# Kernel optimization log

Measured on AMD Instinct MI355X. Metric: run time of the kernel, lower is better.

## Reference

```python
import jax, jax.numpy as jnp
import numpy as np

B, T, C = 4, 2048, 1024
H, DH = 16, 64  # head_count, per-head dim = head_size // head_count


def setup_inputs() -> dict:
    key = jax.random.key(0)
    ks = jax.random.split(key, 5)
    s = 1.0 / np.sqrt(C)
    return {
        "x": jax.random.normal(ks[0], (B, T, C), dtype=jnp.float32),
        "Wq": jax.random.normal(ks[1], (H, C, DH), dtype=jnp.float32) * s,
        "Wk": jax.random.normal(ks[2], (H, C, DH), dtype=jnp.float32) * s,
        "Wv": jax.random.normal(ks[3], (H, C, DH), dtype=jnp.float32) * s,
        "Wproj": jax.random.normal(ks[4], (C, C), dtype=jnp.float32) * s,
    }


def reference(x, Wq, Wk, Wv, Wproj):
    b, t, c = x.shape
    q = jnp.einsum("btc,hcd->bhtd", x, Wq)
    k = jnp.einsum("btc,hcd->bhtd", x, Wk)
    v = jnp.einsum("btc,hcd->bhtd", x, Wv)
    # NOTE: source scales by embed_size**-0.5, not head_dim**-0.5
    wei = jnp.einsum("bhtd,bhsd->bhts", q, k) * (c ** -0.5)
    causal = jnp.tril(jnp.ones((t, t), dtype=bool))
    wei = jnp.where(causal, wei, jnp.finfo(wei.dtype).min)
    wei = jax.nn.softmax(wei, axis=-1)
    out = jnp.einsum("bhts,bhsd->bhtd", wei, v)
    out = out.transpose(0, 2, 1, 3).reshape(b, t, -1)  # concat heads -> [B,T,H*DH]
    return out @ Wproj
```

## Files before the change

kernel.cpp:

```cpp
#include <hip/hip_runtime.h>
#include <math.h>
#include <stdint.h>

#define BB 4
#define TT 2048
#define CC 1024
#define HH 16
#define DH 64
#define BT (BB*TT)
#define NQKV (3*HH*DH)

typedef __attribute__((ext_vector_type(8))) __bf16 bf16x8;
typedef __attribute__((ext_vector_type(4))) float f32x4;
typedef __attribute__((ext_vector_type(16))) float f32x16;
typedef __attribute__((ext_vector_type(8))) unsigned short u16x8;
typedef __attribute__((ext_vector_type(4))) unsigned int u32x4;

__device__ __forceinline__ unsigned short f2b(float f) {
  union { float f; unsigned u; } v; v.f = f;
  unsigned r = v.u + 0x7fffu + ((v.u >> 16) & 1u);
  return (unsigned short)(r >> 16);
}

__device__ __forceinline__ void gload_lds16(const void* g, void* lds) {
  __builtin_amdgcn_global_load_lds(
      (const __attribute__((address_space(1))) void*)(uintptr_t)g,
      (__attribute__((address_space(3))) void*)(uintptr_t)lds, 16, 0, 0);
}

__device__ __forceinline__ unsigned cvtpk_bf16(float lo, float hi) {
  unsigned r;
  asm("v_cvt_pk_bf16_f32 %0, %1, %2" : "=v"(r) : "v"(lo), "v"(hi));
  return r;
}

__device__ __forceinline__ float fexp2(float x) {
#if __has_builtin(__builtin_amdgcn_exp2f)
  return __builtin_amdgcn_exp2f(x);
#else
  float r; asm("v_exp_f32 %0, %1" : "=v"(r) : "v"(x)); return r;
#endif
}

__global__ __launch_bounds__(256) void cvt_bf16(const float* __restrict__ in,
                                                unsigned short* __restrict__ out, int n) {
  int i = (blockIdx.x * 256 + threadIdx.x) * 8;
  if (i + 8 > n) return;
  float4 a = *(const float4*)(in + i);
  float4 b = *(const float4*)(in + i + 4);
  u16x8 pk;
  pk[0] = f2b(a.x); pk[1] = f2b(a.y); pk[2] = f2b(a.z); pk[3] = f2b(a.w);
  pk[4] = f2b(b.x); pk[5] = f2b(b.y); pk[6] = f2b(b.z); pk[7] = f2b(b.w);
  *(u16x8*)(out + i) = pk;
}

__global__ __launch_bounds__(256) void transpose_cvt(const float* __restrict__ in,
                                                     unsigned short* __restrict__ out,
                                                     int R, int Cc) {
  __shared__ float tile[32][33];
  const int z = blockIdx.z;
  in  += (size_t)z * R * Cc;
  out += (size_t)z * R * Cc;
  const int r0 = blockIdx.y * 32, c0 = blockIdx.x * 32;
  const int tx = threadIdx.x, ty = threadIdx.y;
  #pragma unroll
  for (int i = 0; i < 32; i += 8)
    tile[ty + i][tx] = in[(size_t)(r0 + ty + i) * Cc + c0 + tx];
  __syncthreads();
  #pragma unroll
  for (int i = 0; i < 32; i += 8)
    out[(size_t)(c0 + ty + i) * R + r0 + tx] = f2b(tile[tx][ty + i]);
}

template<int MODE>
__global__ __launch_bounds__(256) void mfma_gemm(
    const unsigned short* __restrict__ A,
    const unsigned short* __restrict__ Bt,
    void* __restrict__ Cout, int M, int N, int K)
{
  __shared__ unsigned short As[128 * 32];
  __shared__ unsigned short Bs[128 * 32];
  const int tid = threadIdx.x;
  const int l = tid & 63, w = tid >> 6;
  const int wr = w >> 1, wc = w & 1;
  const long row0 = (long)blockIdx.x * 128, col0 = (long)blockIdx.y * 128;

  const int srow = tid >> 2;
  const int skoff = (tid & 3) * 8;
  const unsigned short* Ap = A + (row0 + srow) * (long)K + skoff;
  const unsigned short* Bp = Bt + (col0 + srow) * (long)K + skoff;
  char* AsB = (char*)As + (size_t)w * 1024;
  char* BsB = (char*)Bs + (size_t)w * 1024;

  f32x4 acc[4][4];
  #pragma unroll
  for (int i = 0; i < 4; ++i)
    #pragma unroll
    for (int j = 0; j < 4; ++j) acc[i][j] = (f32x4){0.f, 0.f, 0.f, 0.f};

  const int fr = l & 15, fg = l >> 4;
  const unsigned short* aBase = As + (wr * 64 + fr) * 32 + fg * 8;
  const unsigned short* bBase = Bs + (wc * 64 + fr) * 32 + fg * 8;

  for (int k0 = 0; k0 < K; k0 += 32) {
    gload_lds16(Ap + k0, AsB);
    gload_lds16(Ap + 64 * (long)K + k0, AsB + 4096);
    gload_lds16(Bp + k0, BsB);
    gload_lds16(Bp + 64 * (long)K + k0, BsB + 4096);
    __syncthreads();
    bf16x8 af[4], bfr[4];
    #pragma unroll
    for (int m = 0; m < 4; ++m) af[m] = *(const bf16x8*)(aBase + m * 16 * 32);
    #pragma unroll
    for (int n = 0; n < 4; ++n) bfr[n] = *(const bf16x8*)(bBase + n * 16 * 32);
    #pragma unroll
    for (int m = 0; m < 4; ++m)
      #pragma unroll
      for (int n = 0; n < 4; ++n)
        acc[m][n] = __builtin_amdgcn_mfma_f32_16x16x32_bf16(af[m], bfr[n], acc[m][n], 0, 0, 0);
    __syncthreads();
  }

  const int fq = l >> 4;
  #pragma unroll
  for (int m = 0; m < 4; ++m) {
    #pragma unroll
    for (int n = 0; n < 4; ++n) {
      #pragma unroll
      for (int r = 0; r < 4; ++r) {
        long grow = row0 + wr * 64 + m * 16 + fq * 4 + r;
        long gcol = col0 + wc * 64 + n * 16 + fr;
        float val = acc[m][n][r];
        if (MODE == 0) {
          int which = (int)(gcol >> 10);
          int h = (int)((gcol >> 6) & 15);
          int d = (int)(gcol & 63);
          int b = (int)(grow >> 11);
          int t = (int)(grow & 2047);
          if (which == 0) val *= 0.04508422017f;
          size_t oi = ((((size_t)which * BB + b) * HH + h) * TT + t) * DH + d;
          ((unsigned short*)Cout)[oi] = f2b(val);
        } else {
          ((float*)Cout)[grow * (long)N + gcol] = val;
        }
      }
    }
  }
}

__device__ __forceinline__ int crow(int r, int hi) { return (r & 3) + 8 * (r >> 2) + 4 * hi; }
__device__ __forceinline__ int vswz(int d) { return ((d & 7) ^ (((d >> 4) & 3) << 1)) << 4; }

__device__ __forceinline__ void swap32(unsigned a, unsigned b, int hi,
                                       unsigned& L, unsigned& H) {
#if __has_builtin(__builtin_amdgcn_permlane32_swap)
  typedef unsigned uint2v __attribute__((ext_vector_type(2)));
  uint2v rr = __builtin_amdgcn_permlane32_swap(a, b, false, false);
  L = rr[0]; H = rr[1];
#else
  unsigned ax = __shfl_xor((int)a, 32, 64), bx = __shfl_xor((int)b, 32, 64);
  L = hi ? bx : a;
  H = hi ? b : ax;
#endif
}

__device__ __forceinline__ void sm_nomax(const f32x16& s, bool diag, int lq, int hi,
                                         float& lsum, bf16x8& pf0, bf16x8& pf1) {
  float p[16];
  #pragma unroll
  for (int r = 0; r < 16; ++r) {
    float e = fexp2(fminf(s[r], 80.f));
    if (diag && (crow(r, hi) > lq)) e = 0.f;
    p[r] = e;
  }
  float t[8];
  #pragma unroll
  for (int r = 0; r < 8; ++r) t[r] = p[r] + p[r + 8];
  #pragma unroll
  for (int r = 0; r < 4; ++r) t[r] = t[r] + t[r + 4];
  lsum += ((t[0] + t[1]) + (t[2] + t[3]));

  unsigned U[4][2];
  #pragma unroll
  for (int g = 0; g < 4; ++g) {
    U[g][0] = cvtpk_bf16(p[4 * g + 0], p[4 * g + 1]);
    U[g][1] = cvtpk_bf16(p[4 * g + 2], p[4 * g + 3]);
  }
  unsigned L0, H0, L1, H1;
  swap32(U[0][0], U[1][0], hi, L0, H0);
  swap32(U[0][1], U[1][1], hi, L1, H1);
  pf0 = __builtin_bit_cast(bf16x8, (u32x4){L0, L1, H0, H1});
  swap32(U[2][0], U[3][0], hi, L0, H0);
  swap32(U[2][1], U[3][1], hi, L1, H1);
  pf1 = __builtin_bit_cast(bf16x8, (u32x4){L0, L1, H0, H1});
}

__global__ __launch_bounds__(256, 2) void attn_mfma(
    const unsigned short* __restrict__ Qb, const unsigned short* __restrict__ Kb,
    const unsigned short* __restrict__ Vb, unsigned short* __restrict__ Ob)
{
  __shared__ unsigned short Ksm[64 * 64];
  __shared__ unsigned short VTsm[64 * 64];

  const int bh = blockIdx.x;
  const int bx = blockIdx.y;
  const int b = bh >> 4, h = bh & 15;
  const int tid = threadIdx.x;
  const int w = tid >> 6, lane = tid & 63;
  const int lq = lane & 31, hi = lane >> 5;
  const int qa0 = bx * 128 + w * 32;
  const int qb0 = (15 - bx) * 128 + w * 32;
  const int ta = qa0 + lq, tb = qb0 + lq;

  const unsigned short* Kp = Kb + (size_t)bh * TT * DH;
  const unsigned short* Vp = Vb + (size_t)bh * TT * DH;

  bf16x8 qfa[4], qfb[4];
  {
    const unsigned short* qpa = Qb + ((size_t)bh * TT + ta) * DH + hi * 8;
    const unsigned short* qpb = Qb + ((size_t)bh * TT + tb) * DH + hi * 8;
    #pragma unroll
    for (int c = 0; c < 4; ++c) {
      qfa[c] = *(const bf16x8*)(qpa + c * 16);
      qfb[c] = *(const bf16x8*)(qpb + c * 16);
    }
  }

  f32x16 accA[2], accB[2];
  #pragma unroll
  for (int dt = 0; dt < 2; ++dt)
    #pragma unroll
    for (int r = 0; r < 16; ++r) { accA[dt][r] = 0.f; accB[dt][r] = 0.f; }
  float lsA = 0.f, lsB = 0.f;

  char* Kc = (char*)Ksm;
  char* Vc = (char*)VTsm;

  const int krow_in = (lane >> 3);
  const int kchunk = (lane & 7) ^ (krow_in & 7);
  char* kdst0 = Kc + w * 2048 + lane * 16;
  char* kdst1 = kdst0 + 1024;

  const int sr = tid >> 2;
  const int sc = (tid & 3) * 16;

  const int ntiles = (15 - bx) * 2 + 2;
  for (int tile = 0; tile < ntiles; ++tile) {
    const int kv0 = tile * 64;
    __syncthreads();
    {
      const unsigned short* kg0 = Kp + (size_t)(kv0 + w * 16 + krow_in) * DH + kchunk * 8;
      gload_lds16(kg0, kdst0);
      gload_lds16(kg0 + 8 * DH, kdst1);
      const unsigned short* vg = Vp + (size_t)(kv0 + sr) * DH + sc;
      u16x8 v0 = *(const u16x8*)vg, v1 = *(const u16x8*)(vg + 8);
      #pragma unroll
      for (int j = 0; j < 8; ++j) {
        int d0 = sc + j, d1 = sc + 8 + j;
        *(unsigned short*)(Vc + ((d0 * 128 + sr * 2) ^ vswz(d0))) = v0[j];
        *(unsigned short*)(Vc + ((d1 * 128 + sr * 2) ^ vswz(d1))) = v1[j];
      }
    }
    __syncthreads();

    #pragma unroll
    for (int sub = 0; sub < 2; ++sub) {
      const int ks = kv0 + sub * 32;
      if (ks > qb0) break;

      const int arow = sub * 32 + lq;
      const int aswz = (arow & 7) << 4;
      bf16x8 kf[4];
      #pragma unroll
      for (int c = 0; c < 4; ++c)
        kf[c] = *(const bf16x8*)(Kc + ((arow * 128 + (c * 16 + hi * 8) * 2) ^ aswz));

      f32x16 s;
      #pragma unroll
      for (int r = 0; r < 16; ++r) s[r] = 0.f;
      __builtin_amdgcn_s_setprio(1);
      #pragma unroll
      for (int c = 0; c < 4; ++c)
        s = __builtin_amdgcn_mfma_f32_32x32x16_bf16(kf[c], qfb[c], s, 0, 0, 0);
      __builtin_amdgcn_s_setprio(0);
      bf16x8 pB0, pB1;
      sm_nomax(s, ks == qb0, lq, hi, lsB, pB0, pB1);

      const bool actA = (ks <= qa0);
      bf16x8 pA0, pA1;
      if (actA) {
        f32x16 s2;
        #pragma unroll
        for (int r = 0; r < 16; ++r) s2[r] = 0.f;
        __builtin_amdgcn_s_setprio(1);
        #pragma unroll
        for (int c = 0; c < 4; ++c)
          s2 = __builtin_amdgcn_mfma_f32_32x32x16_bf16(kf[c], qfa[c], s2, 0, 0, 0);
        __builtin_amdgcn_s_setprio(0);
        sm_nomax(s2, ks == qa0, lq, hi, lsA, pA0, pA1);
      }

      __builtin_amdgcn_s_setprio(1);
      #pragma unroll
      for (int kc = 0; kc < 2; ++kc) {
        bf16x8 pB = kc ? pB1 : pB0;
        bf16x8 pA = kc ? pA1 : pA0;
        #pragma unroll
        for (int dt = 0; dt < 2; ++dt) {
          const int vrow = dt * 32 + lq;
          bf16x8 vf = *(const bf16x8*)(Vc + ((vrow * 128 + (sub * 32 + kc * 16 + hi * 8) * 2) ^ vswz(vrow)));
          accB[dt] = __builtin_amdgcn_mfma_f32_32x32x16_bf16(vf, pB, accB[dt], 0, 0, 0);
          if (actA)
            accA[dt] = __builtin_amdgcn_mfma_f32_32x32x16_bf16(vf, pA, accA[dt], 0, 0, 0);
        }
      }
      __builtin_amdgcn_s_setprio(0);
    }
  }

  {
    const float l = lsA + __shfl_xor(lsA, 32, 64);
    const float inv = 1.f / l;
    unsigned short* op = Ob + ((size_t)b * TT + ta) * CC + h * DH;
    #pragma unroll
    for (int dt = 0; dt < 2; ++dt)
      #pragma unroll
      for (int r = 0; r < 16; ++r)
        op[dt * 32 + crow(r, hi)] = f2b(accA[dt][r] * inv);
  }
  {
    const float l = lsB + __shfl_xor(lsB, 32, 64);
    const float inv = 1.f / l;
    unsigned short* op = Ob + ((size_t)b * TT + tb) * CC + h * DH;
    #pragma unroll
    for (int dt = 0; dt < 2; ++dt)
      #pragma unroll
      for (int r = 0; r < 16; ++r)
        op[dt * 32 + crow(r, hi)] = f2b(accB[dt][r] * inv);
  }
}

extern "C" void kernel_launch(void* const* d_in, const int* in_sizes, int n_in,
                              void* d_out, int out_size, void* d_ws, size_t ws_size,
                              hipStream_t stream) {
  const float* x     = (const float*)d_in[0];
  const float* Wq    = (const float*)d_in[1];
  const float* Wk    = (const float*)d_in[2];
  const float* Wv    = (const float*)d_in[3];
  const float* Wproj = (const float*)d_in[4];

  unsigned short* xb  = (unsigned short*)d_ws;
  unsigned short* Wt  = xb + (size_t)BT * CC;
  unsigned short* WpT = Wt + (size_t)NQKV * CC;
  unsigned short* QKV = WpT + (size_t)CC * CC;
  unsigned short* Ob  = QKV + (size_t)3 * BB * HH * TT * DH;
  unsigned short* Qb  = QKV;
  unsigned short* Kb  = QKV + (size_t)BB * HH * TT * DH;
  unsigned short* Vb  = Kb + (size_t)BB * HH * TT * DH;

  cvt_bf16<<<4096, 256, 0, stream>>>(x, xb, BT * CC);
  dim3 tb(32, 8);
  transpose_cvt<<<dim3(2, 32, 16), tb, 0, stream>>>(Wq, Wt + 0 * (size_t)HH * DH * CC, CC, DH);
  transpose_cvt<<<dim3(2, 32, 16), tb, 0, stream>>>(Wk, Wt + 1 * (size_t)HH * DH * CC, CC, DH);
  transpose_cvt<<<dim3(2, 32, 16), tb, 0, stream>>>(Wv, Wt + 2 * (size_t)HH * DH * CC, CC, DH);
  transpose_cvt<<<dim3(32, 32, 1), tb, 0, stream>>>(Wproj, WpT, CC, CC);

  mfma_gemm<0><<<dim3(64, 24), 256, 0, stream>>>(xb, Wt, QKV, BT, NQKV, CC);
  attn_mfma<<<dim3(64, 8), 256, 0, stream>>>(Qb, Kb, Vb, Ob);
  mfma_gemm<1><<<dim3(64, 8), 256, 0, stream>>>(Ob, WpT, d_out, BT, CC, CC);
}
```

Measured before the change: 201.2 us.

## Pre-transpose V globally and load V^T tiles via direct LDS DMA

Adds a separate kernel that transposes V into a [bh, d, t] layout in the now-free x workspace. The attention kernel can then load V^T tiles with the same swizzled global-to-LDS 16-byte copies used for K, replacing scalar 2-byte scattered LDS stores. The three QKV weight transposes are also merged into one launch. The cost is an extra kernel launch and an extra read and write pass over V.

```diff
diff --git a/kernel.cpp b/kernel.cpp
--- a/kernel.cpp
+++ b/kernel.cpp
@@ -54,13 +54,28 @@
   *(u16x8*)(out + i) = pk;
 }
 
+__global__ __launch_bounds__(256) void transpose_cvt_qkv(
+    const float* __restrict__ Wq, const float* __restrict__ Wk, const float* __restrict__ Wv,
+    unsigned short* __restrict__ out) {
+  __shared__ float tile[32][33];
+  const int z = blockIdx.z;
+  const float* in = (z < 16 ? Wq : (z < 32 ? Wk : Wv)) + (size_t)(z & 15) * CC * DH;
+  unsigned short* o = out + (size_t)z * CC * DH;
+  const int r0 = blockIdx.y * 32, c0 = blockIdx.x * 32;
+  const int tx = threadIdx.x, ty = threadIdx.y;
+  #pragma unroll
+  for (int i = 0; i < 32; i += 8)
+    tile[ty + i][tx] = in[(size_t)(r0 + ty + i) * DH + c0 + tx];
+  __syncthreads();
+  #pragma unroll
+  for (int i = 0; i < 32; i += 8)
+    o[(size_t)(c0 + ty + i) * CC + r0 + tx] = f2b(tile[tx][ty + i]);
+}
+
 __global__ __launch_bounds__(256) void transpose_cvt(const float* __restrict__ in,
                                                      unsigned short* __restrict__ out,
                                                      int R, int Cc) {
   __shared__ float tile[32][33];
-  const int z = blockIdx.z;
-  in  += (size_t)z * R * Cc;
-  out += (size_t)z * R * Cc;
   const int r0 = blockIdx.y * 32, c0 = blockIdx.x * 32;
   const int tx = threadIdx.x, ty = threadIdx.y;
   #pragma unroll
@@ -70,6 +85,26 @@
   #pragma unroll
   for (int i = 0; i < 32; i += 8)
     out[(size_t)(c0 + ty + i) * R + r0 + tx] = f2b(tile[tx][ty + i]);
+}
+
+__global__ __launch_bounds__(256) void vt_transpose(const unsigned short* __restrict__ V,
+                                                    unsigned short* __restrict__ VT) {
+  __shared__ unsigned short t[64][72];
+  const int bh = blockIdx.y;
+  const int t0 = blockIdx.x * 64;
+  const int tid = threadIdx.x;
+  const int r = tid >> 2;
+  const int c = (tid & 3) * 16;
+  const unsigned short* src = V + ((size_t)bh * TT + t0 + r) * DH + c;
+  *(u16x8*)&t[r][c]     = *(const u16x8*)src;
+  *(u16x8*)&t[r][c + 8] = *(const u16x8*)(src + 8);
+  __syncthreads();
+  unsigned short* dst = VT + ((size_t)bh * DH + r) * TT + t0 + c;
+  u16x8 a, b;
+  #pragma unroll
+  for (int j = 0; j < 8; ++j) { a[j] = t[c + j][r]; b[j] = t[c + 8 + j][r]; }
+  *(u16x8*)dst = a;
+  *(u16x8*)(dst + 8) = b;
 }
 
 template<int MODE>
@@ -149,7 +184,6 @@
 }
 
 __device__ __forceinline__ int crow(int r, int hi) { return (r & 3) + 8 * (r >> 2) + 4 * hi; }
-__device__ __forceinline__ int vswz(int d) { return ((d & 7) ^ (((d >> 4) & 3) << 1)) << 4; }
 
 __device__ __forceinline__ void swap32(unsigned a, unsigned b, int hi,
                                        unsigned& L, unsigned& H) {
@@ -197,7 +231,7 @@
 
 __global__ __launch_bounds__(256, 2) void attn_mfma(
     const unsigned short* __restrict__ Qb, const unsigned short* __restrict__ Kb,
-    const unsigned short* __restrict__ Vb, unsigned short* __restrict__ Ob)
+    const unsigned short* __restrict__ VTb, unsigned short* __restrict__ Ob)
 {
   __shared__ unsigned short Ksm[64 * 64];
   __shared__ unsigned short VTsm[64 * 64];
@@ -212,8 +246,8 @@
   const int qb0 = (15 - bx) * 128 + w * 32;
   const int ta = qa0 + lq, tb = qb0 + lq;
 
-  const unsigned short* Kp = Kb + (size_t)bh * TT * DH;
-  const unsigned short* Vp = Vb + (size_t)bh * TT * DH;
+  const unsigned short* Kp  = Kb  + (size_t)bh * TT * DH;
+  const unsigned short* VTp = VTb + (size_t)bh * DH * TT;
 
   bf16x8 qfa[4], qfb[4];
   {
@@ -236,30 +270,21 @@
   char* Kc = (char*)Ksm;
   char* Vc = (char*)VTsm;
 
-  const int krow_in = (lane >> 3);
-  const int kchunk = (lane & 7) ^ (krow_in & 7);
-  char* kdst0 = Kc + w * 2048 + lane * 16;
-  char* kdst1 = kdst0 + 1024;
-
-  const int sr = tid >> 2;
-  const int sc = (tid & 3) * 16;
+  const int srow_in = (lane >> 3);
+  const int schunk = (lane & 7) ^ (srow_in & 7);
+  const int sdoff = w * 2048 + lane * 16;
 
   const int ntiles = (15 - bx) * 2 + 2;
   for (int tile = 0; tile < ntiles; ++tile) {
     const int kv0 = tile * 64;
     __syncthreads();
     {
-      const unsigned short* kg0 = Kp + (size_t)(kv0 + w * 16 + krow_in) * DH + kchunk * 8;
-      gload_lds16(kg0, kdst0);
-      gload_lds16(kg0 + 8 * DH, kdst1);
-      const unsigned short* vg = Vp + (size_t)(kv0 + sr) * DH + sc;
-      u16x8 v0 = *(const u16x8*)vg, v1 = *(const u16x8*)(vg + 8);
-      #pragma unroll
-      for (int j = 0; j < 8; ++j) {
-        int d0 = sc + j, d1 = sc + 8 + j;
-        *(unsigned short*)(Vc + ((d0 * 128 + sr * 2) ^ vswz(d0))) = v0[j];
-        *(unsigned short*)(Vc + ((d1 * 128 + sr * 2) ^ vswz(d1))) = v1[j];
-      }
+      const unsigned short* kg = Kp + (size_t)(kv0 + w * 16 + srow_in) * DH + schunk * 8;
+      gload_lds16(kg, Kc + sdoff);
+      gload_lds16(kg + 8 * DH, Kc + sdoff + 1024);
+      const unsigned short* vg = VTp + (size_t)(w * 16 + srow_in) * TT + kv0 + schunk * 8;
+      gload_lds16(vg, Vc + sdoff);
+      gload_lds16(vg + 8 * TT, Vc + sdoff + 1024);
     }
     __syncthreads();
 
@@ -308,7 +333,7 @@
         #pragma unroll
         for (int dt = 0; dt < 2; ++dt) {
           const int vrow = dt * 32 + lq;
-          bf16x8 vf = *(const bf16x8*)(Vc + ((vrow * 128 + (sub * 32 + kc * 16 + hi * 8) * 2) ^ vswz(vrow)));
+          bf16x8 vf = *(const bf16x8*)(Vc + ((vrow * 128 + sub * 64 + kc * 32 + hi * 16) ^ ((vrow & 7) << 4)));
           accB[dt] = __builtin_amdgcn_mfma_f32_32x32x16_bf16(vf, pB, accB[dt], 0, 0, 0);
           if (actA)
             accA[dt] = __builtin_amdgcn_mfma_f32_32x32x16_bf16(vf, pA, accA[dt], 0, 0, 0);
@@ -357,15 +382,15 @@
   unsigned short* Qb  = QKV;
   unsigned short* Kb  = QKV + (size_t)BB * HH * TT * DH;
   unsigned short* Vb  = Kb + (size_t)BB * HH * TT * DH;
+  unsigned short* VT  = xb;
 
   cvt_bf16<<<4096, 256, 0, stream>>>(x, xb, BT * CC);
   dim3 tb(32, 8);
-  transpose_cvt<<<dim3(2, 32, 16), tb, 0, stream>>>(Wq, Wt + 0 * (size_t)HH * DH * CC, CC, DH);
-  transpose_cvt<<<dim3(2, 32, 16), tb, 0, stream>>>(Wk, Wt + 1 * (size_t)HH * DH * CC, CC, DH);
-  transpose_cvt<<<dim3(2, 32, 16), tb, 0, stream>>>(Wv, Wt + 2 * (size_t)HH * DH * CC, CC, DH);
+  transpose_cvt_qkv<<<dim3(2, 32, 48), tb, 0, stream>>>(Wq, Wk, Wv, Wt);
   transpose_cvt<<<dim3(32, 32, 1), tb, 0, stream>>>(Wproj, WpT, CC, CC);
 
   mfma_gemm<0><<<dim3(64, 24), 256, 0, stream>>>(xb, Wt, QKV, BT, NQKV, CC);
-  attn_mfma<<<dim3(64, 8), 256, 0, stream>>>(Qb, Kb, Vb, Ob);
+  vt_transpose<<<dim3(TT / 64, BB * HH), 256, 0, stream>>>(Vb, VT);
+  attn_mfma<<<dim3(64, 8), 256, 0, stream>>>(Qb, Kb, VT, Ob);
   mfma_gemm<1><<<dim3(64, 8), 256, 0, stream>>>(Ob, WpT, d_out, BT, CC, CC);
 }
```

Measured after the change: 205.4 us. +2.0%, slower.
